# Optimization experiments

Measured on AMD Instinct MI355X. Metric: run time of the kernel, lower is better.

The kernel has to match this reference:

```python
import jax, jax.numpy as jnp
import numpy as np

M_FIELDS = 26   # cin_size[0]
H1 = 128        # cin_size[1]
H2 = 128        # cin_size[2]
BATCH = 2048
EMB_K = 32


def setup_inputs() -> dict:
    key = jax.random.key(0)
    k0, k1, k2, k3, k4 = jax.random.split(key, 5)
    inputs = jax.random.normal(k0, (BATCH, M_FIELDS, EMB_K), dtype=jnp.float32)
    # Conv3d(1, H1, kernel=(26,26,1)) -> weight [H1, H_prev=26, m=26], bias [H1]
    W1 = jax.random.normal(k1, (H1, M_FIELDS, M_FIELDS), dtype=jnp.float32) * 0.05
    b1 = jax.random.normal(k2, (H1,), dtype=jnp.float32) * 0.05
    # Conv3d(1, H2, kernel=(H1,26,1)) -> weight [H2, H1, m=26], bias [H2]
    W2 = jax.random.normal(k3, (H2, H1, M_FIELDS), dtype=jnp.float32) * 0.05
    b2 = jax.random.normal(k4, (H2,), dtype=jnp.float32) * 0.05
    return {"inputs": inputs, "W1": W1, "b1": b1, "W2": W2, "b2": b2}


def _cin_layer(x_prev, x0, W, b):
    # x_prev: [B, H_prev, k], x0: [B, m, k], W: [H, H_prev, m], b: [H]
    # Equivalent to: outer product z[b,i,j,k] = x_prev[b,i,k]*x0[b,j,k],
    # then Conv3d with kernel (H_prev, m, 1): out[b,h,k] = sum_ij W[h,i,j]*z + b[h]
    return jnp.einsum('bik,bjk,hij->bhk', x_prev, x0, W) + b[None, :, None]


def reference(inputs, W1, b1, W2, b2):
    x1 = _cin_layer(inputs, inputs, W1, b1)   # [B, H1, k]
    x2 = _cin_layer(x1, inputs, W2, b2)       # [B, H2, k]
    res = jnp.concatenate([x1, x2], axis=1)   # [B, H1+H2, k]
    return jnp.sum(res, axis=-1)              # [B, H1+H2]
```

## Files before the change

kernel.cpp:

```cpp
#include <hip/hip_runtime.h>

typedef __bf16 bf16;
typedef __bf16 bf16x8 __attribute__((ext_vector_type(8)));
typedef __bf16 bf16x4 __attribute__((ext_vector_type(4)));
typedef float f32x4 __attribute__((ext_vector_type(4)));
typedef unsigned int u32;

#define NB    2048
#define NM    26
#define NJP   27

__device__ __forceinline__ bf16x8 splat8(u32 p) {
  union { u32 u[4]; bf16x8 v; } s;
  s.u[0] = p; s.u[1] = p; s.u[2] = p; s.u[3] = p;
  return s.v;
}

__device__ __forceinline__ u32 dup16(float v) {
  union { bf16 h; unsigned short s; } cv; cv.h = (bf16)v;
  return (u32)cv.s * 0x10001u;
}

__global__ __launch_bounds__(256) void prep_all(
    const float* __restrict__ W1, const float* __restrict__ W2,
    const float* __restrict__ b2,
    bf16* __restrict__ w1t, bf16* __restrict__ w2t2, float* __restrict__ out)
{
  const int bid = blockIdx.x, t = threadIdx.x;
  if (bid < 432) {
    int e = bid*256 + t;
    int el = e & 7, lr = (e >> 3) & 15, lq = (e >> 7) & 3, ni = (e >> 9) & 3;
    int rest = e >> 11;
    int c = rest % NJP, cs_idx = rest / NJP;
    int h = cs_idx*64 + ni*16 + lr;
    int i = lq*8 + el;
    float v = (i < NM && c < NM) ? W1[h*(NM*NM) + i*NM + c] : 0.f;
    w1t[e] = (bf16)v;
  } else if (bid < 2512) {
    int e = (bid-432)*256 + t;
    int el = e & 7, lr = (e >> 3) & 15, lq = (e >> 7) & 3, ni = (e >> 9) & 3;
    int rest = e >> 11;
    int kc = rest % 130, cs_idx = rest / 130;
    int h = cs_idx*64 + ni*16 + lr;
    int c = lq*8 + el;
    float v = (kc < 128 && c < NM) ? W2[h*(128*NM) + kc*NM + c] : 0.f;
    w2t2[e] = (bf16)v;
  } else {
    int e = (bid-2512)*256 + t;
    int b = e >> 7, h = e & 127;
    out[b*256 + 128 + h] = 32.0f * b2[h];
  }
}

#define STEP(CUR, NXT, J) do {                                                 \
  { int jn = ((J)+1 > 25) ? 25 : (J)+1;         \
    sc[NXT][0] = dup16(spw[jn*32]);                                            \
    sc[NXT][1] = dup16(spw[jn*32 + 16]); }                                     \
  _Pragma("unroll")                                                            \
  for (int ni = 0; ni < 4; ++ni)                                               \
    B[NXT][ni] = *(const bf16x8*)(tb + (long)((J)+1)*2048 + ni*512);           \
  _Pragma("unroll")                                                            \
  for (int mi = 0; mi < 2; ++mi) {                                             \
    bf16x8 af = xf[mi] * splat8(sc[CUR][mi]);                                  \
    _Pragma("unroll")                                                          \
    for (int ni = 0; ni < 4; ++ni)                                             \
      acc[mi][ni] = __builtin_amdgcn_mfma_f32_16x16x32_bf16(af, B[CUR][ni],    \
                                                            acc[mi][ni], 0, 0, 0); \
  }                                                                            \
} while (0)

__global__ __launch_bounds__(256, 4) void cin1G(
    const float* __restrict__ in, const bf16* __restrict__ w1t,
    const float* __restrict__ b1, bf16* __restrict__ G2, float* __restrict__ out)
{
  __shared__ __align__(16) bf16 ldsT[4][64*36];
  const int t = threadIdx.x;
  const int lane = t & 63, w = t >> 6;
  const int cs_idx = blockIdx.x & 1, cs = cs_idx * 64;
  const int strip = blockIdx.x >> 1;
  const int bw = strip*4 + w;
  const int lr = lane & 15, lq = lane >> 4;
  const int fo = lq*128 + lr*8;

  const float* bin = in + (long)bw*(NM*32);
  const float* spw = bin + lr;

  bf16x8 xf[2];
  #pragma unroll
  for (int mi = 0; mi < 2; ++mi)
    #pragma unroll
    for (int e = 0; e < 8; ++e) {
      int j = lq*8 + e;
      xf[mi][e] = (bf16)((j < NM) ? bin[j*32 + mi*16 + lr] : 0.f);
    }

  f32x4 acc[2][4];
  #pragma unroll
  for (int mi=0; mi<2; ++mi)
    #pragma unroll
    for (int ni=0; ni<4; ++ni) acc[mi][ni] = {0.f,0.f,0.f,0.f};

  const bf16* tb = w1t + (long)cs_idx*NJP*2048 + fo;

  u32 sc[2][2];
  bf16x8 B[2][4];
  #pragma unroll
  for (int ni = 0; ni < 4; ++ni)
    B[0][ni] = *(const bf16x8*)(tb + ni*512);
  sc[0][0] = dup16(spw[0]);  sc[0][1] = dup16(spw[16]);

  for (int jj = 0; jj < 13; ++jj) {
    STEP(0, 1, 2*jj);
    STEP(1, 0, 2*jj + 1);
  }

  float bias[4];
  #pragma unroll
  for (int ni=0; ni<4; ++ni) bias[ni] = b1[cs + ni*16 + lr];

  #pragma unroll
  for (int ni=0; ni<4; ++ni) {
    float v = 0.f;
    #pragma unroll
    for (int mi=0; mi<2; ++mi)
      #pragma unroll
      for (int r=0; r<4; ++r) v += acc[mi][ni][r];
    v += __shfl_xor(v, 16, 64);
    v += __shfl_xor(v, 32, 64);
    if (lq == 0) out[bw*256 + cs + ni*16 + lr] = v + 32.0f * bias[ni];
  }

  bf16* T = &ldsT[w][0];
  #pragma unroll
  for (int mi=0; mi<2; ++mi)
    #pragma unroll
    for (int ni=0; ni<4; ++ni) {
      bf16x4 pk;
      #pragma unroll
      for (int r=0; r<4; ++r) pk[r] = (bf16)(acc[mi][ni][r] + bias[ni]);
      *(bf16x4*)&T[(ni*16+lr)*36 + mi*16 + lq*4] = pk;
    }

  bf16x8 bg[2];
  #pragma unroll
  for (int nt = 0; nt < 2; ++nt) {
    int j = nt*16 + lr;
    bf16x8 v;
    #pragma unroll
    for (int e=0; e<8; ++e) v[e] = (bf16)0.f;
    if (j < NM) {
      const float* src = bin + j*32 + lq*8;
      f32x4 a = *(const f32x4*)src, c = *(const f32x4*)(src+4);
      #pragma unroll
      for (int e=0; e<4; ++e) { v[e] = (bf16)a[e]; v[4+e] = (bf16)c[e]; }
    }
    bg[nt] = v;
  }
  const long gbase = (long)(bw >> 5)*131072 + (bw & 31)*8;
  #pragma unroll
  for (int mt = 0; mt < 4; ++mt) {
    bf16x8 ag = *(const bf16x8*)&T[(mt*16+lr)*36 + lq*8];
    #pragma unroll
    for (int nt = 0; nt < 2; ++nt) {
      f32x4 z = {0.f,0.f,0.f,0.f};
      f32x4 g = __builtin_amdgcn_mfma_f32_16x16x32_bf16(ag, bg[nt], z, 0, 0, 0);
      const int jh = nt*2 + (lr >> 3), jl = lr & 7;
      #pragma unroll
      for (int r = 0; r < 4; ++r) {
        int i = cs + mt*16 + lq*4 + r;
        G2[gbase + (long)(i*4 + jh)*256 + jl] = (bf16)g[r];
      }
    }
  }
}

#define STEPG(CUR, NXT, KN) do {                                               \
  _Pragma("unroll")                                                            \
  for (int mi = 0; mi < 2; ++mi)                                               \
    A[NXT][mi] = *(const bf16x8*)(Ab + (long)(KN)*1024 + mi*128);              \
  _Pragma("unroll")                                                            \
  for (int ni = 0; ni < 4; ++ni)                                               \
    B[NXT][ni] = *(const bf16x8*)(tb + (long)(KN)*2048 + ni*512);              \
  _Pragma("unroll")                                                            \
  for (int mi = 0; mi < 2; ++mi)                                               \
    _Pragma("unroll")                                                          \
    for (int ni = 0; ni < 4; ++ni)                                             \
      acc[mi][ni] = __builtin_amdgcn_mfma_f32_16x16x32_bf16(A[CUR][mi],        \
                                  B[CUR][ni], acc[CUR?mi:mi][ni], 0, 0, 0);    \
} while (0)

__global__ __launch_bounds__(256, 4) void gemm2(
    const bf16* __restrict__ G2, const bf16* __restrict__ w2t2, float* __restrict__ out)
{
  const int t = threadIdx.x;
  const int lane = t & 63, w = t >> 6;
  const int s = blockIdx.x >> 5;
  const int q32 = blockIdx.x & 31;
  const int tile = q32*4 + w;
  const int cs_idx = tile & 1, ms = tile >> 1;
  const int lr = lane & 15, lq = lane >> 4;
  const int fo = lq*128 + lr*8;
  const int kc0 = s*8;

  const bf16* Ab = G2 + ((long)(ms*512 + lq)*32 + lr)*8;
  const bf16* tb = w2t2 + (long)cs_idx*130*2048 + fo;

  f32x4 acc[2][4];
  #pragma unroll
  for (int mi=0; mi<2; ++mi)
    #pragma unroll
    for (int ni=0; ni<4; ++ni) acc[mi][ni] = {0.f,0.f,0.f,0.f};

  bf16x8 A[2][2], B[2][4];
  #pragma unroll
  for (int mi=0; mi<2; ++mi)
    A[0][mi] = *(const bf16x8*)(Ab + (long)kc0*1024 + mi*128);
  #pragma unroll
  for (int ni=0; ni<4; ++ni)
    B[0][ni] = *(const bf16x8*)(tb + (long)kc0*2048 + ni*512);

  for (int jj = 0; jj < 4; ++jj) {
    STEPG(0, 1, kc0 + 2*jj + 1);
    STEPG(1, 0, kc0 + 2*jj + 2);
  }

  #pragma unroll
  for (int mi=0; mi<2; ++mi)
    #pragma unroll
    for (int ni=0; ni<4; ++ni) {
      int h = cs_idx*64 + ni*16 + lr;
      #pragma unroll
      for (int r=0; r<4; ++r) {
        int b = ms*32 + mi*16 + lq*4 + r;
        atomicAdd(&out[b*256 + 128 + h], acc[mi][ni][r]);
      }
    }
}

extern "C" void kernel_launch(void* const* d_in, const int* in_sizes, int n_in,
                              void* d_out, int out_size, void* d_ws, size_t ws_size,
                              hipStream_t stream) {
  const float* in = (const float*)d_in[0];
  const float* W1 = (const float*)d_in[1];
  const float* b1 = (const float*)d_in[2];
  const float* W2 = (const float*)d_in[3];
  const float* b2 = (const float*)d_in[4];
  float* out = (float*)d_out;

  char* ws = (char*)d_ws;
  bf16* w1t  = (bf16*)(ws);
  bf16* w2t2 = (bf16*)(ws + 1048576);
  bf16* G2   = (bf16*)(ws + 4194304);

  prep_all<<<3536, 256, 0, stream>>>(W1, W2, b2, w1t, w2t2, out);
  cin1G   <<<1024, 256, 0, stream>>>(in, w1t, b1, G2, out);
  gemm2   <<<512,  256, 0, stream>>>(G2, w2t2, out);
}
```

Before: 112.1 us.

## Fuse prep, CIN layer 1 and GEMM2 into one persistent kernel with grid barriers

Replaces three kernel launches with a single 512-block kernel that runs weight prep, the first CIN layer plus G2 construction, and the second GEMM as phases separated by atomic-counter grid barriers. A counter memset is added before the launch. Each block now handles both column halves of layer 1, and GEMM2 tiles are regrouped to 16 rows with a deeper K loop per block. This removes launch gaps and tail effects between stages. In exchange it relies on all 512 blocks being co-resident for the spin barrier, halves parallelism in phase 2, and adds system-scope fence costs.

```diff
diff --git a/kernel.cpp b/kernel.cpp
--- a/kernel.cpp
+++ b/kernel.cpp
@@ -9,6 +9,7 @@
 #define NB    2048
 #define NM    26
 #define NJP   27
+#define NBLK  512
 
 __device__ __forceinline__ bf16x8 splat8(u32 p) {
   union { u32 u[4]; bf16x8 v; } s;
@@ -21,35 +22,16 @@
   return (u32)cv.s * 0x10001u;
 }
 
-__global__ __launch_bounds__(256) void prep_all(
-    const float* __restrict__ W1, const float* __restrict__ W2,
-    const float* __restrict__ b2,
-    bf16* __restrict__ w1t, bf16* __restrict__ w2t2, float* __restrict__ out)
-{
-  const int bid = blockIdx.x, t = threadIdx.x;
-  if (bid < 432) {
-    int e = bid*256 + t;
-    int el = e & 7, lr = (e >> 3) & 15, lq = (e >> 7) & 3, ni = (e >> 9) & 3;
-    int rest = e >> 11;
-    int c = rest % NJP, cs_idx = rest / NJP;
-    int h = cs_idx*64 + ni*16 + lr;
-    int i = lq*8 + el;
-    float v = (i < NM && c < NM) ? W1[h*(NM*NM) + i*NM + c] : 0.f;
-    w1t[e] = (bf16)v;
-  } else if (bid < 2512) {
-    int e = (bid-432)*256 + t;
-    int el = e & 7, lr = (e >> 3) & 15, lq = (e >> 7) & 3, ni = (e >> 9) & 3;
-    int rest = e >> 11;
-    int kc = rest % 130, cs_idx = rest / 130;
-    int h = cs_idx*64 + ni*16 + lr;
-    int c = lq*8 + el;
-    float v = (kc < 128 && c < NM) ? W2[h*(128*NM) + kc*NM + c] : 0.f;
-    w2t2[e] = (bf16)v;
-  } else {
-    int e = (bid-2512)*256 + t;
-    int b = e >> 7, h = e & 127;
-    out[b*256 + 128 + h] = 32.0f * b2[h];
-  }
+__device__ __forceinline__ void grid_barrier(u32* cnt, u32 target) {
+  __syncthreads();
+  if (threadIdx.x == 0) {
+    __threadfence_system();
+    __hip_atomic_fetch_add(cnt, 1u, __ATOMIC_RELEASE, __HIP_MEMORY_SCOPE_SYSTEM);
+    while (__hip_atomic_load(cnt, __ATOMIC_ACQUIRE, __HIP_MEMORY_SCOPE_SYSTEM) < target)
+      __builtin_amdgcn_s_sleep(2);
+    __threadfence_system();
+  }
+  __syncthreads();
 }
 
 #define STEP(CUR, NXT, J) do {                                                 \
@@ -69,172 +51,199 @@
   }                                                                            \
 } while (0)
 
-__global__ __launch_bounds__(256, 4) void cin1G(
-    const float* __restrict__ in, const bf16* __restrict__ w1t,
-    const float* __restrict__ b1, bf16* __restrict__ G2, float* __restrict__ out)
+#define STEPG2(CUR, NXT, KN) do {                                              \
+  A2[NXT] = *(const bf16x8*)(Ab + (long)(KN)*1024);                            \
+  _Pragma("unroll")                                                            \
+  for (int ni = 0; ni < 4; ++ni)                                               \
+    B2[NXT][ni] = *(const bf16x8*)(tbc + (long)(KN)*2048 + ni*512);            \
+  _Pragma("unroll")                                                            \
+  for (int ni = 0; ni < 4; ++ni)                                               \
+    acc2[ni] = __builtin_amdgcn_mfma_f32_16x16x32_bf16(A2[CUR], B2[CUR][ni],   \
+                                                       acc2[ni], 0, 0, 0);     \
+} while (0)
+
+__global__ __launch_bounds__(256, 2) void fused(
+    const float* __restrict__ in, const float* __restrict__ W1,
+    const float* __restrict__ b1, const float* __restrict__ W2,
+    const float* __restrict__ b2, bf16* __restrict__ w1t,
+    bf16* __restrict__ w2t2, bf16* __restrict__ G2, float* __restrict__ out,
+    u32* __restrict__ cnt)
 {
   __shared__ __align__(16) bf16 ldsT[4][64*36];
   const int t = threadIdx.x;
+  const int bid = blockIdx.x;
   const int lane = t & 63, w = t >> 6;
-  const int cs_idx = blockIdx.x & 1, cs = cs_idx * 64;
-  const int strip = blockIdx.x >> 1;
-  const int bw = strip*4 + w;
   const int lr = lane & 15, lq = lane >> 4;
   const int fo = lq*128 + lr*8;
 
-  const float* bin = in + (long)bw*(NM*32);
-  const float* spw = bin + lr;
-
-  bf16x8 xf[2];
   #pragma unroll
-  for (int mi = 0; mi < 2; ++mi)
-    #pragma unroll
-    for (int e = 0; e < 8; ++e) {
-      int j = lq*8 + e;
-      xf[mi][e] = (bf16)((j < NM) ? bin[j*32 + mi*16 + lr] : 0.f);
-    }
-
-  f32x4 acc[2][4];
-  #pragma unroll
-  for (int mi=0; mi<2; ++mi)
-    #pragma unroll
-    for (int ni=0; ni<4; ++ni) acc[mi][ni] = {0.f,0.f,0.f,0.f};
-
-  const bf16* tb = w1t + (long)cs_idx*NJP*2048 + fo;
-
-  u32 sc[2][2];
-  bf16x8 B[2][4];
-  #pragma unroll
-  for (int ni = 0; ni < 4; ++ni)
-    B[0][ni] = *(const bf16x8*)(tb + ni*512);
-  sc[0][0] = dup16(spw[0]);  sc[0][1] = dup16(spw[16]);
-
-  for (int jj = 0; jj < 13; ++jj) {
-    STEP(0, 1, 2*jj);
-    STEP(1, 0, 2*jj + 1);
-  }
-
-  float bias[4];
-  #pragma unroll
-  for (int ni=0; ni<4; ++ni) bias[ni] = b1[cs + ni*16 + lr];
-
-  #pragma unroll
-  for (int ni=0; ni<4; ++ni) {
-    float v = 0.f;
-    #pragma unroll
-    for (int mi=0; mi<2; ++mi)
-      #pragma unroll
-      for (int r=0; r<4; ++r) v += acc[mi][ni][r];
-    v += __shfl_xor(v, 16, 64);
-    v += __shfl_xor(v, 32, 64);
-    if (lq == 0) out[bw*256 + cs + ni*16 + lr] = v + 32.0f * bias[ni];
-  }
-
-  bf16* T = &ldsT[w][0];
-  #pragma unroll
-  for (int mi=0; mi<2; ++mi)
-    #pragma unroll
-    for (int ni=0; ni<4; ++ni) {
-      bf16x4 pk;
-      #pragma unroll
-      for (int r=0; r<4; ++r) pk[r] = (bf16)(acc[mi][ni][r] + bias[ni]);
-      *(bf16x4*)&T[(ni*16+lr)*36 + mi*16 + lq*4] = pk;
-    }
-
-  bf16x8 bg[2];
-  #pragma unroll
-  for (int nt = 0; nt < 2; ++nt) {
-    int j = nt*16 + lr;
-    bf16x8 v;
-    #pragma unroll
-    for (int e=0; e<8; ++e) v[e] = (bf16)0.f;
-    if (j < NM) {
-      const float* src = bin + j*32 + lq*8;
-      f32x4 a = *(const f32x4*)src, c = *(const f32x4*)(src+4);
-      #pragma unroll
-      for (int e=0; e<4; ++e) { v[e] = (bf16)a[e]; v[4+e] = (bf16)c[e]; }
-    }
-    bg[nt] = v;
-  }
-  const long gbase = (long)(bw >> 5)*131072 + (bw & 31)*8;
-  #pragma unroll
-  for (int mt = 0; mt < 4; ++mt) {
-    bf16x8 ag = *(const bf16x8*)&T[(mt*16+lr)*36 + lq*8];
+  for (int g = 0; g < 7; ++g) {
+    int ge = g*131072 + bid*256 + t;
+    if (ge < 110592) {
+      int e = ge;
+      int el = e & 7, plr = (e >> 3) & 15, plq = (e >> 7) & 3, ni = (e >> 9) & 3;
+      int rest = e >> 11;
+      int c = rest % NJP, cs_idx = rest / NJP;
+      int h = cs_idx*64 + ni*16 + plr;
+      int i = plq*8 + el;
+      float v = (i < NM && c < NM) ? W1[h*(NM*NM) + i*NM + c] : 0.f;
+      w1t[e] = (bf16)v;
+    } else if (ge < 643072) {
+      int e = ge - 110592;
+      int el = e & 7, plr = (e >> 3) & 15, plq = (e >> 7) & 3, ni = (e >> 9) & 3;
+      int rest = e >> 11;
+      int kc = rest % 130, cs_idx = rest / 130;
+      int h = cs_idx*64 + ni*16 + plr;
+      int c = plq*8 + el;
+      float v = (kc < 128 && c < NM) ? W2[h*(128*NM) + kc*NM + c] : 0.f;
+      w2t2[e] = (bf16)v;
+    } else if (ge < 905216) {
+      int e = ge - 643072;
+      int b = e >> 7, h = e & 127;
+      out[b*256 + 128 + h] = 32.0f * b2[h];
+    }
+  }
+
+  grid_barrier(cnt, NBLK);
+
+  {
+    const int bw = bid*4 + w;
+    const float* bin = in + (long)bw*(NM*32);
+    const float* spw = bin + lr;
+
+    bf16x8 xf[2];
+    #pragma unroll
+    for (int mi = 0; mi < 2; ++mi)
+      #pragma unroll
+      for (int e = 0; e < 8; ++e) {
+        int j = lq*8 + e;
+        xf[mi][e] = (bf16)((j < NM) ? bin[j*32 + mi*16 + lr] : 0.f);
+      }
+
+    bf16x8 bg[2];
     #pragma unroll
     for (int nt = 0; nt < 2; ++nt) {
-      f32x4 z = {0.f,0.f,0.f,0.f};
-      f32x4 g = __builtin_amdgcn_mfma_f32_16x16x32_bf16(ag, bg[nt], z, 0, 0, 0);
-      const int jh = nt*2 + (lr >> 3), jl = lr & 7;
-      #pragma unroll
-      for (int r = 0; r < 4; ++r) {
-        int i = cs + mt*16 + lq*4 + r;
-        G2[gbase + (long)(i*4 + jh)*256 + jl] = (bf16)g[r];
-      }
-    }
-  }
-}
-
-#define STEPG(CUR, NXT, KN) do {                                               \
-  _Pragma("unroll")                                                            \
-  for (int mi = 0; mi < 2; ++mi)                                               \
-    A[NXT][mi] = *(const bf16x8*)(Ab + (long)(KN)*1024 + mi*128);              \
-  _Pragma("unroll")                                                            \
-  for (int ni = 0; ni < 4; ++ni)                                               \
-    B[NXT][ni] = *(const bf16x8*)(tb + (long)(KN)*2048 + ni*512);              \
-  _Pragma("unroll")                                                            \
-  for (int mi = 0; mi < 2; ++mi)                                               \
-    _Pragma("unroll")                                                          \
-    for (int ni = 0; ni < 4; ++ni)                                             \
-      acc[mi][ni] = __builtin_amdgcn_mfma_f32_16x16x32_bf16(A[CUR][mi],        \
-                                  B[CUR][ni], acc[CUR?mi:mi][ni], 0, 0, 0);    \
-} while (0)
-
-__global__ __launch_bounds__(256, 4) void gemm2(
-    const bf16* __restrict__ G2, const bf16* __restrict__ w2t2, float* __restrict__ out)
-{
-  const int t = threadIdx.x;
-  const int lane = t & 63, w = t >> 6;
-  const int s = blockIdx.x >> 5;
-  const int q32 = blockIdx.x & 31;
-  const int tile = q32*4 + w;
-  const int cs_idx = tile & 1, ms = tile >> 1;
-  const int lr = lane & 15, lq = lane >> 4;
-  const int fo = lq*128 + lr*8;
-  const int kc0 = s*8;
-
-  const bf16* Ab = G2 + ((long)(ms*512 + lq)*32 + lr)*8;
-  const bf16* tb = w2t2 + (long)cs_idx*130*2048 + fo;
-
-  f32x4 acc[2][4];
-  #pragma unroll
-  for (int mi=0; mi<2; ++mi)
-    #pragma unroll
-    for (int ni=0; ni<4; ++ni) acc[mi][ni] = {0.f,0.f,0.f,0.f};
-
-  bf16x8 A[2][2], B[2][4];
-  #pragma unroll
-  for (int mi=0; mi<2; ++mi)
-    A[0][mi] = *(const bf16x8*)(Ab + (long)kc0*1024 + mi*128);
-  #pragma unroll
-  for (int ni=0; ni<4; ++ni)
-    B[0][ni] = *(const bf16x8*)(tb + (long)kc0*2048 + ni*512);
-
-  for (int jj = 0; jj < 4; ++jj) {
-    STEPG(0, 1, kc0 + 2*jj + 1);
-    STEPG(1, 0, kc0 + 2*jj + 2);
-  }
-
-  #pragma unroll
-  for (int mi=0; mi<2; ++mi)
+      int j = nt*16 + lr;
+      bf16x8 v;
+      #pragma unroll
+      for (int e=0; e<8; ++e) v[e] = (bf16)0.f;
+      if (j < NM) {
+        const float* src = bin + j*32 + lq*8;
+        f32x4 a = *(const f32x4*)src, c = *(const f32x4*)(src+4);
+        #pragma unroll
+        for (int e=0; e<4; ++e) { v[e] = (bf16)a[e]; v[4+e] = (bf16)c[e]; }
+      }
+      bg[nt] = v;
+    }
+
+    const long gbase = (long)(bw >> 5)*131072 + (bw & 31)*8;
+    bf16* T = &ldsT[w][0];
+
+    for (int csi = 0; csi < 2; ++csi) {
+      const int cs = csi * 64;
+
+      f32x4 acc[2][4];
+      #pragma unroll
+      for (int mi=0; mi<2; ++mi)
+        #pragma unroll
+        for (int ni=0; ni<4; ++ni) acc[mi][ni] = {0.f,0.f,0.f,0.f};
+
+      const bf16* tb = w1t + (long)csi*NJP*2048 + fo;
+
+      u32 sc[2][2];
+      bf16x8 B[2][4];
+      #pragma unroll
+      for (int ni = 0; ni < 4; ++ni)
+        B[0][ni] = *(const bf16x8*)(tb + ni*512);
+      sc[0][0] = dup16(spw[0]);  sc[0][1] = dup16(spw[16]);
+
+      for (int jj = 0; jj < 13; ++jj) {
+        STEP(0, 1, 2*jj);
+        STEP(1, 0, 2*jj + 1);
+      }
+
+      float bias[4];
+      #pragma unroll
+      for (int ni=0; ni<4; ++ni) bias[ni] = b1[cs + ni*16 + lr];
+
+      #pragma unroll
+      for (int ni=0; ni<4; ++ni) {
+        float v = 0.f;
+        #pragma unroll
+        for (int mi=0; mi<2; ++mi)
+          #pragma unroll
+          for (int r=0; r<4; ++r) v += acc[mi][ni][r];
+        v += __shfl_xor(v, 16, 64);
+        v += __shfl_xor(v, 32, 64);
+        if (lq == 0) out[bw*256 + cs + ni*16 + lr] = v + 32.0f * bias[ni];
+      }
+
+      #pragma unroll
+      for (int mi=0; mi<2; ++mi)
+        #pragma unroll
+        for (int ni=0; ni<4; ++ni) {
+          bf16x4 pk;
+          #pragma unroll
+          for (int r=0; r<4; ++r) pk[r] = (bf16)(acc[mi][ni][r] + bias[ni]);
+          *(bf16x4*)&T[(ni*16+lr)*36 + mi*16 + lq*4] = pk;
+        }
+
+      #pragma unroll
+      for (int mt = 0; mt < 4; ++mt) {
+        bf16x8 ag = *(const bf16x8*)&T[(mt*16+lr)*36 + lq*8];
+        #pragma unroll
+        for (int nt = 0; nt < 2; ++nt) {
+          f32x4 z = {0.f,0.f,0.f,0.f};
+          f32x4 gq = __builtin_amdgcn_mfma_f32_16x16x32_bf16(ag, bg[nt], z, 0, 0, 0);
+          const int jh = nt*2 + (lr >> 3), jl = lr & 7;
+          #pragma unroll
+          for (int r = 0; r < 4; ++r) {
+            int i = cs + mt*16 + lq*4 + r;
+            G2[gbase + (long)(i*4 + jh)*256 + jl] = (bf16)gq[r];
+          }
+        }
+      }
+    }
+  }
+
+  grid_barrier(cnt, 2*NBLK);
+
+  {
+    const int s = bid >> 6;
+    const int q64 = bid & 63;
+    const int tile = q64*4 + w;
+    const int cs_idx = tile & 1, ms16 = tile >> 1;
+    const int ms = ms16 >> 1, mif = ms16 & 1;
+    const int kc0 = s*16;
+
+    const bf16* Ab  = G2 + ((long)(ms*512 + lq)*32 + lr)*8 + mif*128;
+    const bf16* tbc = w2t2 + (long)cs_idx*130*2048 + fo;
+
+    f32x4 acc2[4];
+    #pragma unroll
+    for (int ni=0; ni<4; ++ni) acc2[ni] = {0.f,0.f,0.f,0.f};
+
+    bf16x8 A2[2], B2[2][4];
+    A2[0] = *(const bf16x8*)(Ab + (long)kc0*1024);
+    #pragma unroll
+    for (int ni=0; ni<4; ++ni)
+      B2[0][ni] = *(const bf16x8*)(tbc + (long)kc0*2048 + ni*512);
+
+    for (int jj = 0; jj < 8; ++jj) {
+      STEPG2(0, 1, kc0 + 2*jj + 1);
+      STEPG2(1, 0, kc0 + 2*jj + 2);
+    }
+
     #pragma unroll
     for (int ni=0; ni<4; ++ni) {
       int h = cs_idx*64 + ni*16 + lr;
       #pragma unroll
       for (int r=0; r<4; ++r) {
-        int b = ms*32 + mi*16 + lq*4 + r;
-        atomicAdd(&out[b*256 + 128 + h], acc[mi][ni][r]);
-      }
-    }
+        int b = ms16*16 + lq*4 + r;
+        atomicAdd(&out[b*256 + 128 + h], acc2[ni][r]);
+      }
+    }
+  }
 }
 
 extern "C" void kernel_launch(void* const* d_in, const int* in_sizes, int n_in,
@@ -250,9 +259,9 @@
   char* ws = (char*)d_ws;
   bf16* w1t  = (bf16*)(ws);
   bf16* w2t2 = (bf16*)(ws + 1048576);
+  u32*  cnt  = (u32*) (ws + 3145728);
   bf16* G2   = (bf16*)(ws + 4194304);
 
-  prep_all<<<3536, 256, 0, stream>>>(W1, W2, b2, w1t, w2t2, out);
-  cin1G   <<<1024, 256, 0, stream>>>(in, w1t, b1, G2, out);
-  gemm2   <<<512,  256, 0, stream>>>(G2, w2t2, out);
-}
+  hipMemsetAsync(cnt, 0, 64, stream);
+  fused<<<NBLK, 256, 0, stream>>>(in, W1, b1, W2, b2, w1t, w2t2, G2, out, cnt);
+}
```

Result: slower. 267.8 us (+139.0%).

## Vectorize G2 stores, remap block order, fold bias init into gemm2

Applied to the files above, without the earlier changes.

The G2 intermediate is now written as packed bf16x4 stores. This is done by swapping the MFMA operands so each lane holds consecutive output elements, replacing the previous scattered 2-byte stores. Block indices in cin1G and gemm2 are remapped so that neighbouring blocks share rows or weight slices, which should improve L2 reuse. The weight-prep kernel becomes a 628-block grid-stride loop and no longer writes the 32*b2 bias into out; instead the s==0 split of gemm2 adds the bias before its atomicAdd. That removes the 3536-block prep launch, but the second half of out now depends on being zero before gemm2's atomics, and nothing in this code clears it.

```diff
diff --git a/kernel.cpp b/kernel.cpp
--- a/kernel.cpp
+++ b/kernel.cpp
@@ -23,32 +23,31 @@
 
 __global__ __launch_bounds__(256) void prep_all(
     const float* __restrict__ W1, const float* __restrict__ W2,
-    const float* __restrict__ b2,
-    bf16* __restrict__ w1t, bf16* __restrict__ w2t2, float* __restrict__ out)
+    bf16* __restrict__ w1t, bf16* __restrict__ w2t2)
 {
   const int bid = blockIdx.x, t = threadIdx.x;
-  if (bid < 432) {
-    int e = bid*256 + t;
-    int el = e & 7, lr = (e >> 3) & 15, lq = (e >> 7) & 3, ni = (e >> 9) & 3;
-    int rest = e >> 11;
-    int c = rest % NJP, cs_idx = rest / NJP;
-    int h = cs_idx*64 + ni*16 + lr;
-    int i = lq*8 + el;
-    float v = (i < NM && c < NM) ? W1[h*(NM*NM) + i*NM + c] : 0.f;
-    w1t[e] = (bf16)v;
-  } else if (bid < 2512) {
-    int e = (bid-432)*256 + t;
-    int el = e & 7, lr = (e >> 3) & 15, lq = (e >> 7) & 3, ni = (e >> 9) & 3;
-    int rest = e >> 11;
-    int kc = rest % 130, cs_idx = rest / 130;
-    int h = cs_idx*64 + ni*16 + lr;
-    int c = lq*8 + el;
-    float v = (kc < 128 && c < NM) ? W2[h*(128*NM) + kc*NM + c] : 0.f;
-    w2t2[e] = (bf16)v;
-  } else {
-    int e = (bid-2512)*256 + t;
-    int b = e >> 7, h = e & 127;
-    out[b*256 + 128 + h] = 32.0f * b2[h];
+  #pragma unroll
+  for (int g = 0; g < 4; ++g) {
+    int ge = g*160768 + bid*256 + t;
+    if (ge < 110592) {
+      int e = ge;
+      int el = e & 7, lr = (e >> 3) & 15, lq = (e >> 7) & 3, ni = (e >> 9) & 3;
+      int rest = e >> 11;
+      int c = rest % NJP, cs_idx = rest / NJP;
+      int h = cs_idx*64 + ni*16 + lr;
+      int i = lq*8 + el;
+      float v = (i < NM && c < NM) ? W1[h*(NM*NM) + i*NM + c] : 0.f;
+      w1t[e] = (bf16)v;
+    } else {
+      int e = ge - 110592;
+      int el = e & 7, lr = (e >> 3) & 15, lq = (e >> 7) & 3, ni = (e >> 9) & 3;
+      int rest = e >> 11;
+      int kc = rest % 130, cs_idx = rest / 130;
+      int h = cs_idx*64 + ni*16 + lr;
+      int c = lq*8 + el;
+      float v = (kc < 128 && c < NM) ? W2[h*(128*NM) + kc*NM + c] : 0.f;
+      w2t2[e] = (bf16)v;
+    }
   }
 }
 
@@ -75,12 +74,16 @@
 {
   __shared__ __align__(16) bf16 ldsT[4][64*36];
   const int t = threadIdx.x;
+  const int bid = blockIdx.x;
   const int lane = t & 63, w = t >> 6;
-  const int cs_idx = blockIdx.x & 1, cs = cs_idx * 64;
-  const int strip = blockIdx.x >> 1;
-  const int bw = strip*4 + w;
+  const int x = bid & 7, u = bid >> 3;
+  const int m8 = (u >> 4)*8 + x;
+  const int v = u & 15;
+  const int strip = m8*8 + (v >> 1);
+  const int cs_idx = v & 1, cs = cs_idx * 64;
   const int lr = lane & 15, lq = lane >> 4;
   const int fo = lq*128 + lr*8;
+  const int bw = strip*4 + w;
 
   const float* bin = in + (long)bw*(NM*32);
   const float* spw = bin + lr;
@@ -120,14 +123,14 @@
 
   #pragma unroll
   for (int ni=0; ni<4; ++ni) {
-    float v = 0.f;
+    float vv = 0.f;
     #pragma unroll
     for (int mi=0; mi<2; ++mi)
       #pragma unroll
-      for (int r=0; r<4; ++r) v += acc[mi][ni][r];
-    v += __shfl_xor(v, 16, 64);
-    v += __shfl_xor(v, 32, 64);
-    if (lq == 0) out[bw*256 + cs + ni*16 + lr] = v + 32.0f * bias[ni];
+      for (int r=0; r<4; ++r) vv += acc[mi][ni][r];
+    vv += __shfl_xor(vv, 16, 64);
+    vv += __shfl_xor(vv, 32, 64);
+    if (lq == 0) out[bw*256 + cs + ni*16 + lr] = vv + 32.0f * bias[ni];
   }
 
   bf16* T = &ldsT[w][0];
@@ -145,16 +148,16 @@
   #pragma unroll
   for (int nt = 0; nt < 2; ++nt) {
     int j = nt*16 + lr;
-    bf16x8 v;
-    #pragma unroll
-    for (int e=0; e<8; ++e) v[e] = (bf16)0.f;
+    bf16x8 vv;
+    #pragma unroll
+    for (int e=0; e<8; ++e) vv[e] = (bf16)0.f;
     if (j < NM) {
       const float* src = bin + j*32 + lq*8;
       f32x4 a = *(const f32x4*)src, c = *(const f32x4*)(src+4);
       #pragma unroll
-      for (int e=0; e<4; ++e) { v[e] = (bf16)a[e]; v[4+e] = (bf16)c[e]; }
-    }
-    bg[nt] = v;
+      for (int e=0; e<4; ++e) { vv[e] = (bf16)a[e]; vv[4+e] = (bf16)c[e]; }
+    }
+    bg[nt] = vv;
   }
   const long gbase = (long)(bw >> 5)*131072 + (bw & 31)*8;
   #pragma unroll
@@ -163,13 +166,12 @@
     #pragma unroll
     for (int nt = 0; nt < 2; ++nt) {
       f32x4 z = {0.f,0.f,0.f,0.f};
-      f32x4 g = __builtin_amdgcn_mfma_f32_16x16x32_bf16(ag, bg[nt], z, 0, 0, 0);
-      const int jh = nt*2 + (lr >> 3), jl = lr & 7;
-      #pragma unroll
-      for (int r = 0; r < 4; ++r) {
-        int i = cs + mt*16 + lq*4 + r;
-        G2[gbase + (long)(i*4 + jh)*256 + jl] = (bf16)g[r];
-      }
+      f32x4 g = __builtin_amdgcn_mfma_f32_16x16x32_bf16(bg[nt], ag, z, 0, 0, 0);
+      bf16x4 pk;
+      #pragma unroll
+      for (int r = 0; r < 4; ++r) pk[r] = (bf16)g[r];
+      const int kh = (cs + mt*16 + lr)*4 + nt*2 + (lq >> 1);
+      *(bf16x4*)&G2[gbase + (long)kh*256 + (lq & 1)*4] = pk;
     }
   }
 }
@@ -180,30 +182,32 @@
     A[NXT][mi] = *(const bf16x8*)(Ab + (long)(KN)*1024 + mi*128);              \
   _Pragma("unroll")                                                            \
   for (int ni = 0; ni < 4; ++ni)                                               \
-    B[NXT][ni] = *(const bf16x8*)(tb + (long)(KN)*2048 + ni*512);              \
+    B[NXT][ni] = *(const bf16x8*)(tbc + (long)(KN)*2048 + ni*512);             \
   _Pragma("unroll")                                                            \
   for (int mi = 0; mi < 2; ++mi)                                               \
     _Pragma("unroll")                                                          \
     for (int ni = 0; ni < 4; ++ni)                                             \
       acc[mi][ni] = __builtin_amdgcn_mfma_f32_16x16x32_bf16(A[CUR][mi],        \
-                                  B[CUR][ni], acc[CUR?mi:mi][ni], 0, 0, 0);    \
+                                  B[CUR][ni], acc[mi][ni], 0, 0, 0);           \
 } while (0)
 
 __global__ __launch_bounds__(256, 4) void gemm2(
-    const bf16* __restrict__ G2, const bf16* __restrict__ w2t2, float* __restrict__ out)
+    const bf16* __restrict__ G2, const bf16* __restrict__ w2t2,
+    const float* __restrict__ b2, float* __restrict__ out)
 {
   const int t = threadIdx.x;
   const int lane = t & 63, w = t >> 6;
   const int s = blockIdx.x >> 5;
   const int q32 = blockIdx.x & 31;
-  const int tile = q32*4 + w;
-  const int cs_idx = tile & 1, ms = tile >> 1;
+  const int x = q32 & 7, q = q32 >> 3;
+  const int ms = x + q*16 + (w >> 1)*8;
+  const int cs_idx = w & 1;
   const int lr = lane & 15, lq = lane >> 4;
   const int fo = lq*128 + lr*8;
   const int kc0 = s*8;
 
-  const bf16* Ab = G2 + ((long)(ms*512 + lq)*32 + lr)*8;
-  const bf16* tb = w2t2 + (long)cs_idx*130*2048 + fo;
+  const bf16* Ab  = G2 + ((long)(ms*512 + lq)*32 + lr)*8;
+  const bf16* tbc = w2t2 + (long)cs_idx*130*2048 + fo;
 
   f32x4 acc[2][4];
   #pragma unroll
@@ -217,11 +221,22 @@
     A[0][mi] = *(const bf16x8*)(Ab + (long)kc0*1024 + mi*128);
   #pragma unroll
   for (int ni=0; ni<4; ++ni)
-    B[0][ni] = *(const bf16x8*)(tb + (long)kc0*2048 + ni*512);
+    B[0][ni] = *(const bf16x8*)(tbc + (long)kc0*2048 + ni*512);
 
   for (int jj = 0; jj < 4; ++jj) {
     STEPG(0, 1, kc0 + 2*jj + 1);
     STEPG(1, 0, kc0 + 2*jj + 2);
+  }
+
+  if (s == 0) {
+    #pragma unroll
+    for (int ni=0; ni<4; ++ni) {
+      float bv = 32.0f * b2[cs_idx*64 + ni*16 + lr];
+      #pragma unroll
+      for (int mi=0; mi<2; ++mi)
+        #pragma unroll
+        for (int r=0; r<4; ++r) acc[mi][ni][r] += bv;
+    }
   }
 
   #pragma unroll
@@ -252,7 +267,7 @@
   bf16* w2t2 = (bf16*)(ws + 1048576);
   bf16* G2   = (bf16*)(ws + 4194304);
 
-  prep_all<<<3536, 256, 0, stream>>>(W1, W2, b2, w1t, w2t2, out);
+  prep_all<<<628,  256, 0, stream>>>(W1, W2, w1t, w2t2);
   cin1G   <<<1024, 256, 0, stream>>>(in, w1t, b1, G2, out);
-  gemm2   <<<512,  256, 0, stream>>>(G2, w2t2, out);
-}
+  gemm2   <<<512,  256, 0, stream>>>(G2, w2t2, b2, out);
+}
```

Measured after the change: 112.8 us. Within noise of the previous version (+0.7%).
